# Kernel tuning notes

Measured on AMD Instinct MI355X. Metric: run time of the kernel, lower is better.

## Reference

```python
import jax, jax.numpy as jnp
import numpy as np

D_HEAD = 128
N_HEADS = 8
BATCH = 8
SEQ = 1024


def setup_inputs() -> dict:
    key = jax.random.key(0)
    ks = jax.random.split(key, 11)
    d, nh = D_HEAD, N_HEADS
    D = nh * d
    s_in = 1.0 / np.sqrt(d)   # torch Linear default init bound, fan_in=d
    s_out = 1.0 / np.sqrt(D)  # fan_in=D for out_proj
    u = lambda k, shape, s: jax.random.uniform(k, shape, jnp.float32, -s, s)
    return {
        "q": jax.random.normal(ks[0], (BATCH, SEQ, d), jnp.float32),
        "k": jax.random.normal(ks[1], (BATCH, SEQ, d), jnp.float32),
        "v": jax.random.normal(ks[2], (BATCH, SEQ, d), jnp.float32),
        "Wq": u(ks[3], (d, D), s_in), "bq": u(ks[4], (D,), s_in),
        "Wk": u(ks[5], (d, D), s_in), "bk": u(ks[6], (D,), s_in),
        "Wv": u(ks[7], (d, D), s_in), "bv": u(ks[8], (D,), s_in),
        "Wo": u(ks[9], (D, d), s_out), "bo": u(ks[10], (d,), s_out),
    }


def reference(q, k, v, Wq, bq, Wk, bk, Wv, bv, Wo, bo):
    B, T, d_in = q.shape
    S = k.shape[1]
    nh = N_HEADS
    # projections: [B, L, nh*d] -> [B, nh, L, d]
    split = lambda x: x.reshape(x.shape[0], x.shape[1], nh, -1).transpose(0, 2, 1, 3)
    qh = split(q @ Wq + bq)
    kh = split(k @ Wk + bk)
    vh = split(v @ Wv + bv)
    d_head = qh.shape[-1]
    # scaled dot-product scores: [B, nh, T, S]
    scores = jnp.einsum('bhtd,bhsd->bhts', qh, kh) / jnp.sqrt(jnp.float32(d_head))
    # causal mask (future positions -> -inf), matches triu(fill(-inf), 1)
    causal = jnp.triu(jnp.ones((T, S), dtype=bool), 1)
    scores = jnp.where(causal[None, None], -jnp.inf, scores)
    # softmax in float32 then cast back, as the original does
    probs = jax.nn.softmax(scores.astype(jnp.float32), axis=-1).astype(scores.dtype)
    o = jnp.einsum('bhts,bhsd->bhtd', probs, vh)          # [B, nh, T, d]
    o = o.transpose(0, 2, 1, 3).reshape(B, T, nh * d_head)  # [B, T, D]
    return o @ Wo + bo                                     # [B, T, d]
```

## Files before the change

### kernel.cpp

```cpp
#include <hip/hip_runtime.h>
#include <hip/hip_bf16.h>


typedef __attribute__((ext_vector_type(8))) short short8;
typedef __attribute__((ext_vector_type(4))) short short4v;
typedef __attribute__((ext_vector_type(4))) float f32x4;

#define B_   8
#define S_   1024
#define DH_  128
#define NH_  8
#define DM_  1024

#define MFMA16(a, b, c) __builtin_amdgcn_mfma_f32_16x16x32_bf16((a), (b), (c), 0, 0, 0)

#define GLOAD_LDS16(gsrc, ldst)                                              \
  __builtin_amdgcn_global_load_lds(                                          \
      (const __attribute__((address_space(1))) void*)(gsrc),                 \
      (__attribute__((address_space(3))) void*)(ldst), 16, 0, 0)

__device__ __forceinline__ float bf2f(unsigned short u) {
  union { unsigned int i; float f; } x; x.i = ((unsigned int)u) << 16; return x.f;
}
__device__ __forceinline__ unsigned short f2bf(float f) {
  union { float f; unsigned int i; } x; x.f = f;
  unsigned int r = (x.i + 0x7fffu + ((x.i >> 16) & 1u)) >> 16;
  return (unsigned short)r;
}
__device__ __forceinline__ unsigned short f2h(float f) {
  union { _Float16 h; unsigned short u; } x; x.h = (_Float16)f; return x.u;
}
__device__ __forceinline__ float h2f(unsigned short u) {
  union { unsigned short u; _Float16 h; } x; x.u = u; return (float)x.h;
}
__device__ __forceinline__ float ldany(const void* p, int i, int fp) {
  return fp ? ((const float*)p)[i] : bf2f(((const unsigned short*)p)[i]);
}

__global__ void k_detect(const unsigned short* __restrict__ in, int* __restrict__ flag) {
  __shared__ int f;
  int tid = threadIdx.x;
  if (tid == 0) f = 0;
  __syncthreads();
  int t = 0;
  for (int i = tid; i < 16384; i += 256) {
    unsigned h = in[i];
    unsigned e = (h >> 7) & 0xFFu, m = h & 0x7Fu;
    if (e == 0xFFu || (e == 0u && m != 0u)) t = 1;
  }
  if (t) atomicOr(&f, 1);
  __syncthreads();
  if (tid == 0) *flag = f;
}

__global__ void k_cvt_x(const void* __restrict__ q, const void* __restrict__ k,
                        const void* __restrict__ v, const int* __restrict__ flag,
                        unsigned short* __restrict__ Xq, unsigned short* __restrict__ Xk,
                        unsigned short* __restrict__ Xv) {
  const int fp = *flag;
  int z = blockIdx.y;
  const void* in = (z == 0) ? q : (z == 1) ? k : v;
  unsigned short* out = (z == 0) ? Xq : (z == 1) ? Xk : Xv;
  int e4 = (blockIdx.x * 256 + threadIdx.x) * 4;
  if (fp) {
    f32x4 x = *(const f32x4*)&((const float*)in)[e4];
    short4v o;
#pragma unroll
    for (int j = 0; j < 4; ++j) o[j] = (short)f2bf(x[j]);
    *(short4v*)&out[e4] = o;
  } else {
    *(short4v*)&out[e4] = *(const short4v*)&((const unsigned short*)in)[e4];
  }
}

__global__ void k_cvt_w(const void* __restrict__ Wq, const void* __restrict__ Wk,
                        const void* __restrict__ Wv, const void* __restrict__ Wo,
                        const void* __restrict__ bq, const void* __restrict__ bk,
                        const void* __restrict__ bv, const void* __restrict__ bo,
                        const int* __restrict__ flag,
                        unsigned short* __restrict__ wqT, unsigned short* __restrict__ wkT,
                        unsigned short* __restrict__ wvT, unsigned short* __restrict__ woT,
                        unsigned short* __restrict__ bqc, unsigned short* __restrict__ bkc,
                        unsigned short* __restrict__ bvc, unsigned short* __restrict__ boc) {
  const int fp = *flag;
  int g = blockIdx.x * 256 + threadIdx.x;
  if (g < 393216) {
    int z = g >> 17, e = g & 131071;
    const void* in = (z == 0) ? Wq : (z == 1) ? Wk : Wv;
    unsigned short* out = (z == 0) ? wqT : (z == 1) ? wkT : wvT;
    int r = e >> 10, c = e & 1023;
    out[c * 128 + r] = f2bf(ldany(in, e, fp));
  } else if (g < 524288) {
    int e = g - 393216;
    int r = e >> 7, c = e & 127;
    woT[c * 1024 + r] = f2bf(ldany(Wo, e, fp));
  } else if (g < 525312) {
    int e = g - 524288; bqc[e] = f2bf(ldany(bq, e, fp));
  } else if (g < 526336) {
    int e = g - 525312; bkc[e] = f2bf(ldany(bk, e, fp));
  } else if (g < 527360) {
    int e = g - 526336; bvc[e] = f2bf(ldany(bv, e, fp));
  } else if (g < 527488) {
    int e = g - 527360; boc[e] = f2bf(ldany(bo, e, fp));
  }
}

__global__ __launch_bounds__(256) void k_qkv(
    const unsigned short* __restrict__ Xq, const unsigned short* __restrict__ Xk,
    const unsigned short* __restrict__ Xv,
    const unsigned short* __restrict__ WqT, const unsigned short* __restrict__ WkT,
    const unsigned short* __restrict__ WvT,
    const unsigned short* __restrict__ bq, const unsigned short* __restrict__ bk,
    const unsigned short* __restrict__ bv,
    unsigned short* __restrict__ Qp, unsigned short* __restrict__ Kp,
    unsigned short* __restrict__ VpT) {
  __shared__ unsigned short vtile[128][136];

  const int mat = blockIdx.z;
  const unsigned short* X    = (mat == 0) ? Xq  : (mat == 1) ? Xk  : Xv;
  const unsigned short* WT   = (mat == 0) ? WqT : (mat == 1) ? WkT : WvT;
  const unsigned short* bias = (mat == 0) ? bq  : (mat == 1) ? bk  : bv;
  const float scale = (mat == 0) ? (1.4426950408889634f / 11.313708498984761f) : 1.0f;

  const int tid = threadIdx.x, lane = tid & 63, wave = tid >> 6;
  const int wm = wave >> 1, wn = wave & 1;
  const int l15 = lane & 15, lg = lane >> 4;
  const int mbase = blockIdx.x * 128 + wm * 64;
  const int nbase = blockIdx.y * 128 + wn * 64;

  short8 a[4][4];
#pragma unroll
  for (int mi = 0; mi < 4; ++mi)
#pragma unroll
    for (int kk = 0; kk < 4; ++kk)
      a[mi][kk] = *(const short8*)&X[(mbase + mi * 16 + l15) * DH_ + kk * 32 + lg * 8];

  f32x4 acc[4][4];
#pragma unroll
  for (int mi = 0; mi < 4; ++mi)
#pragma unroll
    for (int ni = 0; ni < 4; ++ni) acc[mi][ni] = (f32x4){0.f, 0.f, 0.f, 0.f};

#pragma unroll
  for (int ni = 0; ni < 4; ++ni) {
    short8 bfr[4];
#pragma unroll
    for (int kk = 0; kk < 4; ++kk)
      bfr[kk] = *(const short8*)&WT[(nbase + ni * 16 + l15) * DH_ + kk * 32 + lg * 8];
#pragma unroll
    for (int mi = 0; mi < 4; ++mi)
#pragma unroll
      for (int kk = 0; kk < 4; ++kk)
        acc[mi][ni] = MFMA16(a[mi][kk], bfr[kk], acc[mi][ni]);
  }

  if (mat < 2) {
    unsigned short* Out = (mat == 0) ? Qp : Kp;
#pragma unroll
    for (int mi = 0; mi < 4; ++mi)
#pragma unroll
      for (int ni = 0; ni < 4; ++ni) {
        int n = nbase + ni * 16 + l15;
        float bv_ = bf2f(bias[n]);
        int h = n >> 7, dh = n & 127;
#pragma unroll
        for (int reg = 0; reg < 4; ++reg) {
          int m = mbase + mi * 16 + lg * 4 + reg;
          int b = m >> 10, t = m & 1023;
          float val = (acc[mi][ni][reg] + bv_) * scale;
          Out[((b * NH_ + h) * S_ + t) * DH_ + dh] = f2bf(val);
        }
      }
  } else {
#pragma unroll
    for (int mi = 0; mi < 4; ++mi)
#pragma unroll
      for (int ni = 0; ni < 4; ++ni) {
        int nl = wn * 64 + ni * 16 + l15;
        float bv_ = bf2f(bias[blockIdx.y * 128 + nl]);
#pragma unroll
        for (int reg = 0; reg < 4; ++reg) {
          int ml_ = wm * 64 + mi * 16 + lg * 4 + reg;
          vtile[ml_][nl] = f2bf(acc[mi][ni][reg] + bv_);
        }
      }
    __syncthreads();
    int n = tid >> 1;
    int thalf = (tid & 1) * 64;
    int b = blockIdx.x >> 3;
    int h = blockIdx.y;
    int base = ((b * NH_ + h) * DH_ + n) * S_ + (blockIdx.x & 7) * 128 + thalf;
#pragma unroll
    for (int jj = 0; jj < 8; ++jj) {
      short8 v;
#pragma unroll
      for (int j2 = 0; j2 < 8; ++j2) v[j2] = (short)vtile[thalf + jj * 8 + j2][n];
      *(short8*)&VpT[base + jj * 8] = v;
    }
  }
}

__global__ __launch_bounds__(256) void k_attn_split(
    const unsigned short* __restrict__ Qp, const unsigned short* __restrict__ Kp,
    const unsigned short* __restrict__ VpT,
    unsigned short* __restrict__ Opart, float* __restrict__ ml,
    unsigned short* __restrict__ O) {
  __shared__ __align__(16) unsigned short kbuf[2][4096];
  __shared__ __align__(16) unsigned short vbuf[2][4096];
  __shared__ __align__(16) unsigned short plds[4][16][44];

  const int tid = threadIdx.x, lane = tid & 63, w = tid >> 6;
  const int l15 = lane & 15, lg = lane >> 4;

  const int bid = blockIdx.x;
  const int swz = (bid & 7) * 320 + (bid >> 3);
  const int bh = swz / 40;
  const int bj = 39 - (swz % 40);
  int G, c;
  if (bj < 4)       { G = bj;                  c = 0; }
  else if (bj < 12) { G = 4 + ((bj - 4) >> 1); c = (bj - 4) & 1; }
  else if (bj < 24) { G = 8 + (bj - 12) / 3;   c = (bj - 12) % 3; }
  else              { G = 12 + ((bj - 24) >> 2); c = (bj - 24) & 3; }
  const int qw = 4 * G + w;
  const int q0 = qw * 16;
  const int cd = G >> 2;
  const bool dia = (c == cd);
  const int sbeg = c * 256;
  const int nt_w   = dia ? ((qw >> 1) + 1 - 8 * c) : 8;
  const int nt_blk = dia ? (2 * G + 2 - 8 * c) : 8;

  const unsigned short* Qb = Qp + bh * (S_ * DH_);
  const unsigned short* Kb = Kp + bh * (S_ * DH_);
  const unsigned short* Vb = VpT + bh * (DH_ * S_);

  const int krow4 = lane >> 4;
  const int kslot = lane & 15;
  const int vd16  = lane >> 2;
  const int vslot = lane & 3;

#define STAGE(bb, sb_) do {                                                        \
    int r0_ = w * 8 + krow4;                                                       \
    GLOAD_LDS16(Kb + ((sb_) + r0_) * DH_ + ((kslot ^ (r0_ & 7)) * 8),              \
                &kbuf[bb][(w * 8) * 128]);                                         \
    int r1_ = w * 8 + 4 + krow4;                                                   \
    GLOAD_LDS16(Kb + ((sb_) + r1_) * DH_ + ((kslot ^ (r1_ & 7)) * 8),              \
                &kbuf[bb][(w * 8 + 4) * 128]);                                     \
    int d0_ = w * 32 + vd16;                                                       \
    GLOAD_LDS16(Vb + d0_ * S_ + (sb_) + vslot * 8, &vbuf[bb][(w * 32) * 32]);      \
    int d1_ = w * 32 + 16 + vd16;                                                  \
    GLOAD_LDS16(Vb + d1_ * S_ + (sb_) + vslot * 8, &vbuf[bb][(w * 32 + 16) * 32]); \
  } while (0)

  short8 qf[4];
#pragma unroll
  for (int kk = 0; kk < 4; ++kk)
    qf[kk] = *(const short8*)&Qb[(q0 + l15) * DH_ + kk * 32 + lg * 8];

  short8 ones;
#pragma unroll
  for (int jj = 0; jj < 8; ++jj) ones[jj] = (short)0x3F80;

  f32x4 of[8], l_acc;
  float m_[4];
#pragma unroll
  for (int di = 0; di < 8; ++di) of[di] = (f32x4){0.f, 0.f, 0.f, 0.f};
  l_acc = (f32x4){0.f, 0.f, 0.f, 0.f};
#pragma unroll
  for (int reg = 0; reg < 4; ++reg) m_[reg] = -1e30f;

  STAGE(0, sbeg);
  __syncthreads();

  for (int kt = 0; kt < nt_blk; ++kt) {
    const int cb = kt & 1;
    if (kt + 1 < nt_blk) STAGE(cb ^ 1, sbeg + (kt + 1) * 32);

    if (kt < nt_w) {
      const int sb = sbeg + kt * 32;
      const int xsl = l15 & 7;

      f32x4 s0 = (f32x4){0.f, 0.f, 0.f, 0.f}, s1 = (f32x4){0.f, 0.f, 0.f, 0.f};
#pragma unroll
      for (int kk = 0; kk < 4; ++kk) {
        short8 kf0 = *(const short8*)&kbuf[cb][l15 * 128 + (((kk * 4 + lg) ^ xsl) * 8)];
        short8 kf1 = *(const short8*)&kbuf[cb][(16 + l15) * 128 + (((kk * 4 + lg) ^ xsl) * 8)];
        s0 = MFMA16(qf[kk], kf0, s0);
        s1 = MFMA16(qf[kk], kf1, s1);
      }

      if (dia && kt == nt_w - 1) {
        const int qrow = q0 + lg * 4;
#pragma unroll
        for (int reg = 0; reg < 4; ++reg) {
          if (sb + l15 > qrow + reg)      s0[reg] = -1e30f;
          if (sb + 16 + l15 > qrow + reg) s1[reg] = -1e30f;
        }
      }

      bool need = false;
      float vmax[4];
#pragma unroll
      for (int reg = 0; reg < 4; ++reg) {
        vmax[reg] = fmaxf(s0[reg], s1[reg]);
        need |= (vmax[reg] > m_[reg] + 8.0f);
      }
      if (__any(need)) {
        float alpha[4];
#pragma unroll
        for (int reg = 0; reg < 4; ++reg) {
          float rm = vmax[reg];
#pragma unroll
          for (int d = 1; d < 16; d <<= 1) rm = fmaxf(rm, __shfl_xor(rm, d));
          float mn = fmaxf(m_[reg], rm);
          alpha[reg] = __builtin_amdgcn_exp2f(m_[reg] - mn);
          m_[reg] = mn;
        }
#pragma unroll
        for (int di = 0; di < 8; ++di)
#pragma unroll
          for (int reg = 0; reg < 4; ++reg) of[di][reg] *= alpha[reg];
#pragma unroll
        for (int reg = 0; reg < 4; ++reg) l_acc[reg] *= alpha[reg];
      }

#pragma unroll
      for (int reg = 0; reg < 4; ++reg) {
        float p0 = __builtin_amdgcn_exp2f(s0[reg] - m_[reg]);
        float p1 = __builtin_amdgcn_exp2f(s1[reg] - m_[reg]);
        union { float f; unsigned int i; } u0, u1;
        u0.f = p0; u1.f = p1;
        plds[w][lg * 4 + reg][l15]      = (unsigned short)((u0.i + 0x8000u) >> 16);
        plds[w][lg * 4 + reg][16 + l15] = (unsigned short)((u1.i + 0x8000u) >> 16);
      }

      short8 pa = *(const short8*)&plds[w][l15][lg * 8];

#pragma unroll
      for (int di = 0; di < 8; ++di) {
        short8 vfd = *(const short8*)&vbuf[cb][(di * 16 + l15) * 32 + lg * 8];
        of[di] = MFMA16(pa, vfd, of[di]);
      }
      l_acc = MFMA16(pa, ones, l_acc);
    }
    __syncthreads();
  }

  if (qw < 16) {
    const int b = bh >> 3, h = bh & 7;
#pragma unroll
    for (int reg = 0; reg < 4; ++reg) {
      int row = lg * 4 + reg;
      float inv = 1.0f / l_acc[reg];
      int qq = q0 + row;
#pragma unroll
      for (int di = 0; di < 8; ++di)
        O[(b * S_ + qq) * DM_ + h * DH_ + di * 16 + l15] = f2bf(of[di][reg] * inv);
    }
  } else {
    int runit;
    if (qw < 32)      runit = 16 + 2 * (qw - 16) + c;
    else if (qw < 48) runit = 48 + 3 * (qw - 32) + c;
    else              runit = 96 + 4 * (qw - 48) + c;
    const int g = bh * 160 + runit;
    unsigned short* op = Opart + g * 2048;
    float* mlg = ml + g * 32;
#pragma unroll
    for (int reg = 0; reg < 4; ++reg) {
      int row = lg * 4 + reg;
      float inv = 1.0f / l_acc[reg];
#pragma unroll
      for (int di = 0; di < 8; ++di)
        op[row * 128 + di * 16 + l15] = f2h(of[di][reg] * inv);
      if (l15 == 0) {
        mlg[row * 2]     = m_[reg];
        mlg[row * 2 + 1] = l_acc[reg];
      }
    }
  }
#undef STAGE
}

__global__ void k_combine(const unsigned short* __restrict__ Opart,
                          const float* __restrict__ ml,
                          unsigned short* __restrict__ O) {
  const int bh = blockIdx.x / 48, qw = 16 + blockIdx.x % 48;
  const int nc = (qw >> 4) + 1;
  const int rbase = (qw < 32) ? 16 + 2 * (qw - 16)
                  : (qw < 48) ? 48 + 3 * (qw - 32)
                              : 96 + 4 * (qw - 48);
  const int g0 = bh * 160 + rbase;
  const int tid = threadIdx.x;
  const int row = tid >> 4, d0 = (tid & 15) * 8;

  float m[4], l[4];
  float mx = -1e30f;
  for (int i = 0; i < nc; ++i) {
    m[i] = ml[(g0 + i) * 32 + row * 2];
    l[i] = ml[(g0 + i) * 32 + row * 2 + 1];
    mx = fmaxf(mx, m[i]);
  }
  float wt[4], wsum = 0.f;
  for (int i = 0; i < nc; ++i) { wt[i] = l[i] * exp2f(m[i] - mx); wsum += wt[i]; }
  float invw = 1.0f / wsum;

  float acc[8];
#pragma unroll
  for (int jj = 0; jj < 8; ++jj) acc[jj] = 0.f;
  for (int i = 0; i < nc; ++i) {
    short8 v = *(const short8*)&Opart[(g0 + i) * 2048 + row * 128 + d0];
    float wgt = wt[i];
#pragma unroll
    for (int jj = 0; jj < 8; ++jj) acc[jj] += wgt * h2f((unsigned short)v[jj]);
  }

  const int b = bh >> 3, h = bh & 7;
  const int qq = qw * 16 + row;
  short8 o;
#pragma unroll
  for (int jj = 0; jj < 8; ++jj) o[jj] = (short)f2bf(acc[jj] * invw);
  *(short8*)&O[(b * S_ + qq) * DM_ + h * DH_ + d0] = o;
}

__global__ __launch_bounds__(256) void k_attn(
    const unsigned short* __restrict__ Qp, const unsigned short* __restrict__ Kp,
    const unsigned short* __restrict__ VpT, unsigned short* __restrict__ O) {
  __shared__ __align__(16) unsigned short plds[4][2][16][44];

  const int qt = 7 - blockIdx.x;
  const int bh = blockIdx.y;
  const int tid = threadIdx.x, lane = tid & 63, w = tid >> 6;
  const int l15 = lane & 15, lg = lane >> 4;
  const int q0 = qt * 128 + w * 32;

  const unsigned short* Qb = Qp + bh * (S_ * DH_);
  const unsigned short* Kb = Kp + bh * (S_ * DH_);
  const unsigned short* Vb = VpT + bh * (DH_ * S_);

  short8 qf[2][4];
#pragma unroll
  for (int mi = 0; mi < 2; ++mi)
#pragma unroll
    for (int kk = 0; kk < 4; ++kk)
      qf[mi][kk] = *(const short8*)&Qb[(q0 + mi * 16 + l15) * DH_ + kk * 32 + lg * 8];

  f32x4 of[2][8];
  float m_[2][4], l_[2][4];
#pragma unroll
  for (int mi = 0; mi < 2; ++mi) {
#pragma unroll
    for (int di = 0; di < 8; ++di) of[mi][di] = (f32x4){0.f, 0.f, 0.f, 0.f};
#pragma unroll
    for (int reg = 0; reg < 4; ++reg) { m_[mi][reg] = -1e30f; l_[mi][reg] = 0.f; }
  }

  const int ntiles = q0 / 32 + 1;
  for (int kt = 0; kt < ntiles; ++kt) {
    const int sb = kt * 32;
    const bool lastt = (kt == ntiles - 1);

    f32x4 s[2][2];
#pragma unroll
    for (int mi = 0; mi < 2; ++mi)
#pragma unroll
      for (int ni = 0; ni < 2; ++ni) s[mi][ni] = (f32x4){0.f, 0.f, 0.f, 0.f};
#pragma unroll
    for (int ni = 0; ni < 2; ++ni) {
      short8 kf[4];
#pragma unroll
      for (int kk = 0; kk < 4; ++kk)
        kf[kk] = *(const short8*)&Kb[(sb + ni * 16 + l15) * DH_ + kk * 32 + lg * 8];
#pragma unroll
      for (int mi = 0; mi < 2; ++mi)
#pragma unroll
        for (int kk = 0; kk < 4; ++kk)
          s[mi][ni] = MFMA16(qf[mi][kk], kf[kk], s[mi][ni]);
    }

#pragma unroll
    for (int mi = 0; mi < 2; ++mi) {
      float alpha[4];
#pragma unroll
      for (int reg = 0; reg < 4; ++reg) {
        int q = q0 + mi * 16 + lg * 4 + reg;
        float v0 = s[mi][0][reg];
        float v1 = s[mi][1][reg];
        if (lastt) {
          if (sb + l15 > q)      v0 = -1e30f;
          if (sb + 16 + l15 > q) v1 = -1e30f;
        }
        float rmax = fmaxf(v0, v1);
#pragma unroll
        for (int d = 1; d < 16; d <<= 1) rmax = fmaxf(rmax, __shfl_xor(rmax, d));
        float mn = fmaxf(m_[mi][reg], rmax);
        alpha[reg] = __builtin_amdgcn_exp2f(m_[mi][reg] - mn);
        m_[mi][reg] = mn;
        float p0 = __builtin_amdgcn_exp2f(v0 - mn), p1 = __builtin_amdgcn_exp2f(v1 - mn);
        float rs = p0 + p1;
#pragma unroll
        for (int d = 1; d < 16; d <<= 1) rs += __shfl_xor(rs, d);
        l_[mi][reg] = l_[mi][reg] * alpha[reg] + rs;
        plds[w][mi][lg * 4 + reg][l15]      = f2bf(p0);
        plds[w][mi][lg * 4 + reg][16 + l15] = f2bf(p1);
      }
#pragma unroll
      for (int di = 0; di < 8; ++di)
#pragma unroll
        for (int reg = 0; reg < 4; ++reg) of[mi][di][reg] *= alpha[reg];
    }

    short8 pa[2];
#pragma unroll
    for (int mi = 0; mi < 2; ++mi)
      pa[mi] = *(const short8*)&plds[w][mi][l15][lg * 8];

#pragma unroll
    for (int di = 0; di < 8; ++di) {
      short8 vf = *(const short8*)&Vb[(di * 16 + l15) * S_ + sb + lg * 8];
#pragma unroll
      for (int mi = 0; mi < 2; ++mi) of[mi][di] = MFMA16(pa[mi], vf, of[mi][di]);
    }
  }

  const int b = bh >> 3, h = bh & 7;
#pragma unroll
  for (int mi = 0; mi < 2; ++mi)
#pragma unroll
    for (int reg = 0; reg < 4; ++reg) {
      float inv = 1.0f / l_[mi][reg];
      int q = q0 + mi * 16 + lg * 4 + reg;
#pragma unroll
      for (int di = 0; di < 8; ++di) {
        int d = di * 16 + l15;
        O[(b * S_ + q) * DM_ + h * DH_ + d] = f2bf(of[mi][di][reg] * inv);
      }
    }
}

__global__ __launch_bounds__(256) void k_oproj(
    const unsigned short* __restrict__ O, const unsigned short* __restrict__ WoT,
    float* __restrict__ outacc) {
  const int tid = threadIdx.x, lane = tid & 63, wave = tid >> 6;
  const int wm = wave >> 1, wn = wave & 1;
  const int l15 = lane & 15, lg = lane >> 4;
  const int mbase = blockIdx.x * 128 + wm * 64;
  const int kc = blockIdx.y;

  f32x4 acc[4][4];
#pragma unroll
  for (int mi = 0; mi < 4; ++mi)
#pragma unroll
    for (int ni = 0; ni < 4; ++ni) acc[mi][ni] = (f32x4){0.f, 0.f, 0.f, 0.f};

  for (int ks = 0; ks < 8; ++ks) {
    int kb = kc * 256 + ks * 32;
    short8 a[4], bfr[4];
#pragma unroll
    for (int mi = 0; mi < 4; ++mi)
      a[mi] = *(const short8*)&O[(mbase + mi * 16 + l15) * DM_ + kb + lg * 8];
#pragma unroll
    for (int ni = 0; ni < 4; ++ni)
      bfr[ni] = *(const short8*)&WoT[(wn * 64 + ni * 16 + l15) * DM_ + kb + lg * 8];
#pragma unroll
    for (int mi = 0; mi < 4; ++mi)
#pragma unroll
      for (int ni = 0; ni < 4; ++ni) acc[mi][ni] = MFMA16(a[mi], bfr[ni], acc[mi][ni]);
  }

  float* oa = outacc + kc * (8192 * 128);
#pragma unroll
  for (int mi = 0; mi < 4; ++mi)
#pragma unroll
    for (int ni = 0; ni < 4; ++ni) {
      int n = wn * 64 + ni * 16 + l15;
#pragma unroll
      for (int reg = 0; reg < 4; ++reg) {
        int m = mbase + mi * 16 + lg * 4 + reg;
        oa[m * 128 + n] = acc[mi][ni][reg];
      }
    }
}

__global__ void k_final(const float* __restrict__ outacc,
                        const unsigned short* __restrict__ boc,
                        const int* __restrict__ flag, void* __restrict__ out) {
  int i4 = (blockIdx.x * 256 + threadIdx.x) * 4;
  f32x4 v = *(const f32x4*)&outacc[i4];
  v += *(const f32x4*)&outacc[1048576 + i4];
  v += *(const f32x4*)&outacc[2097152 + i4];
  v += *(const f32x4*)&outacc[3145728 + i4];
  int n0 = i4 & 127;
#pragma unroll
  for (int j = 0; j < 4; ++j) v[j] += bf2f(boc[n0 + j]);
  if (*flag) {
    *(f32x4*)&((float*)out)[i4] = v;
  } else {
    short4v o;
#pragma unroll
    for (int j = 0; j < 4; ++j) o[j] = (short)f2bf(v[j]);
    *(short4v*)&((unsigned short*)out)[i4] = o;
  }
}

extern "C" void kernel_launch(void* const* d_in, const int* in_sizes, int n_in,
                              void* d_out, int out_size, void* d_ws, size_t ws_size,
                              hipStream_t stream) {
  const void* q  = d_in[0];
  const void* k  = d_in[1];
  const void* v  = d_in[2];
  const void* Wq = d_in[3];
  const void* bq = d_in[4];
  const void* Wk = d_in[5];
  const void* bk = d_in[6];
  const void* Wv = d_in[7];
  const void* bv = d_in[8];
  const void* Wo = d_in[9];
  const void* bo = d_in[10];

  char* ws = (char*)d_ws;
  int*            flag = (int*)(ws + 0);
  unsigned short* wqT  = (unsigned short*)(ws + 4096);
  unsigned short* wkT  = (unsigned short*)(ws + 266240);
  unsigned short* wvT  = (unsigned short*)(ws + 528384);
  unsigned short* woT  = (unsigned short*)(ws + 790528);
  unsigned short* bqc  = (unsigned short*)(ws + 1052672);
  unsigned short* bkc  = (unsigned short*)(ws + 1054720);
  unsigned short* bvc  = (unsigned short*)(ws + 1056768);
  unsigned short* boc  = (unsigned short*)(ws + 1058816);
  unsigned short* Xq   = (unsigned short*)(ws + 2097152);
  unsigned short* Xk   = (unsigned short*)(ws + 4194304);
  unsigned short* Xv   = (unsigned short*)(ws + 6291456);
  unsigned short* Qp   = (unsigned short*)(ws + 8388608);
  unsigned short* Kp   = (unsigned short*)(ws + 25165824);
  unsigned short* VpT  = (unsigned short*)(ws + 41943040);
  unsigned short* O    = (unsigned short*)(ws + 58720256);
  float*          oacc = (float*)(ws + 75497472);
  unsigned short* Opart= (unsigned short*)(ws + 75497472);
  float*          ml   = (float*)(ws + 2097152);

  const bool use_split = ws_size >= (size_t)117440512;

  k_detect<<<dim3(1), 256, 0, stream>>>((const unsigned short*)q, flag);
  k_cvt_x<<<dim3(1024, 3), 256, 0, stream>>>(q, k, v, flag, Xq, Xk, Xv);
  k_cvt_w<<<dim3(2061), 256, 0, stream>>>(Wq, Wk, Wv, Wo, bq, bk, bv, bo, flag,
                                          wqT, wkT, wvT, woT, bqc, bkc, bvc, boc);
  k_qkv<<<dim3(64, 8, 3), 256, 0, stream>>>(Xq, Xk, Xv, wqT, wkT, wvT, bqc, bkc, bvc,
                                            Qp, Kp, VpT);
  if (use_split) {
    k_attn_split<<<dim3(2560), 256, 0, stream>>>(Qp, Kp, VpT, Opart, ml, O);
    k_combine<<<dim3(3072), 256, 0, stream>>>(Opart, ml, O);
  } else {
    k_attn<<<dim3(8, 64), 256, 0, stream>>>(Qp, Kp, VpT, O);
  }
  k_oproj<<<dim3(64, 4), 256, 0, stream>>>(O, woT, oacc);
  k_final<<<dim3(1024), 256, 0, stream>>>(oacc, boc, flag, d_out);
}
```

Measured before the change: 142.5 us.

## Stage Q/K projection output through LDS, prefetch weights, set MFMA priority

The QKV projection now writes every matrix's biased and scaled tile into shared memory and stores Q/K with 16-byte coalesced vector writes, replacing scattered 2-byte global stores. Weight fragments are double-buffered so the next column group loads while the current MFMAs run. The attention kernels raise wave priority around MFMA loops with s_setprio, and the P staging row pitch changes from 44 to 48 elements. This adds a barrier and LDS traffic to the Q/K path, and the new pitch may change LDS bank conflicts.

Result: no change. 144.6 us (+1.5%).

```diff
diff --git a/kernel.cpp b/kernel.cpp
--- a/kernel.cpp
+++ b/kernel.cpp
@@ -114,7 +114,7 @@
     const unsigned short* __restrict__ bv,
     unsigned short* __restrict__ Qp, unsigned short* __restrict__ Kp,
     unsigned short* __restrict__ VpT) {
-  __shared__ unsigned short vtile[128][136];
+  __shared__ __align__(16) unsigned short vtile[128][136];
 
   const int mat = blockIdx.z;
   const unsigned short* X    = (mat == 0) ? Xq  : (mat == 1) ? Xk  : Xv;
@@ -141,54 +141,55 @@
 #pragma unroll
     for (int ni = 0; ni < 4; ++ni) acc[mi][ni] = (f32x4){0.f, 0.f, 0.f, 0.f};
 
+  short8 bfr[2][4];
+#pragma unroll
+  for (int kk = 0; kk < 4; ++kk)
+    bfr[0][kk] = *(const short8*)&WT[(nbase + l15) * DH_ + kk * 32 + lg * 8];
+
 #pragma unroll
   for (int ni = 0; ni < 4; ++ni) {
-    short8 bfr[4];
-#pragma unroll
-    for (int kk = 0; kk < 4; ++kk)
-      bfr[kk] = *(const short8*)&WT[(nbase + ni * 16 + l15) * DH_ + kk * 32 + lg * 8];
+    if (ni < 3) {
+#pragma unroll
+      for (int kk = 0; kk < 4; ++kk)
+        bfr[(ni + 1) & 1][kk] =
+            *(const short8*)&WT[(nbase + (ni + 1) * 16 + l15) * DH_ + kk * 32 + lg * 8];
+    }
 #pragma unroll
     for (int mi = 0; mi < 4; ++mi)
 #pragma unroll
       for (int kk = 0; kk < 4; ++kk)
-        acc[mi][ni] = MFMA16(a[mi][kk], bfr[kk], acc[mi][ni]);
-  }
-
+        acc[mi][ni] = MFMA16(a[mi][kk], bfr[ni & 1][kk], acc[mi][ni]);
+  }
+
+#pragma unroll
+  for (int mi = 0; mi < 4; ++mi)
+#pragma unroll
+    for (int ni = 0; ni < 4; ++ni) {
+      int nl = wn * 64 + ni * 16 + l15;
+      float bv_ = bf2f(bias[blockIdx.y * 128 + nl]);
+#pragma unroll
+      for (int reg = 0; reg < 4; ++reg) {
+        int ml_ = wm * 64 + mi * 16 + lg * 4 + reg;
+        vtile[ml_][nl] = f2bf((acc[mi][ni][reg] + bv_) * scale);
+      }
+    }
+  __syncthreads();
+
+  const int b = blockIdx.x >> 3;
+  const int h = blockIdx.y;
   if (mat < 2) {
-    unsigned short* Out = (mat == 0) ? Qp : Kp;
-#pragma unroll
-    for (int mi = 0; mi < 4; ++mi)
-#pragma unroll
-      for (int ni = 0; ni < 4; ++ni) {
-        int n = nbase + ni * 16 + l15;
-        float bv_ = bf2f(bias[n]);
-        int h = n >> 7, dh = n & 127;
-#pragma unroll
-        for (int reg = 0; reg < 4; ++reg) {
-          int m = mbase + mi * 16 + lg * 4 + reg;
-          int b = m >> 10, t = m & 1023;
-          float val = (acc[mi][ni][reg] + bv_) * scale;
-          Out[((b * NH_ + h) * S_ + t) * DH_ + dh] = f2bf(val);
-        }
-      }
+    unsigned short* Out = ((mat == 0) ? Qp : Kp) +
+        ((b * NH_ + h) * S_ + (blockIdx.x & 7) * 128) * DH_;
+#pragma unroll
+    for (int j = 0; j < 8; ++j) {
+      int r = j * 16 + (tid >> 4);
+      int c0 = (tid & 15) * 8;
+      short8 v = *(const short8*)&vtile[r][c0];
+      *(short8*)&Out[j * 2048 + tid * 8] = v;
+    }
   } else {
-#pragma unroll
-    for (int mi = 0; mi < 4; ++mi)
-#pragma unroll
-      for (int ni = 0; ni < 4; ++ni) {
-        int nl = wn * 64 + ni * 16 + l15;
-        float bv_ = bf2f(bias[blockIdx.y * 128 + nl]);
-#pragma unroll
-        for (int reg = 0; reg < 4; ++reg) {
-          int ml_ = wm * 64 + mi * 16 + lg * 4 + reg;
-          vtile[ml_][nl] = f2bf(acc[mi][ni][reg] + bv_);
-        }
-      }
-    __syncthreads();
     int n = tid >> 1;
     int thalf = (tid & 1) * 64;
-    int b = blockIdx.x >> 3;
-    int h = blockIdx.y;
     int base = ((b * NH_ + h) * DH_ + n) * S_ + (blockIdx.x & 7) * 128 + thalf;
 #pragma unroll
     for (int jj = 0; jj < 8; ++jj) {
@@ -207,7 +208,7 @@
     unsigned short* __restrict__ O) {
   __shared__ __align__(16) unsigned short kbuf[2][4096];
   __shared__ __align__(16) unsigned short vbuf[2][4096];
-  __shared__ __align__(16) unsigned short plds[4][16][44];
+  __shared__ __align__(16) unsigned short plds[4][16][48];
 
   const int tid = threadIdx.x, lane = tid & 63, w = tid >> 6;
   const int l15 = lane & 15, lg = lane >> 4;
@@ -280,6 +281,7 @@
       const int xsl = l15 & 7;
 
       f32x4 s0 = (f32x4){0.f, 0.f, 0.f, 0.f}, s1 = (f32x4){0.f, 0.f, 0.f, 0.f};
+      __builtin_amdgcn_s_setprio(1);
 #pragma unroll
       for (int kk = 0; kk < 4; ++kk) {
         short8 kf0 = *(const short8*)&kbuf[cb][l15 * 128 + (((kk * 4 + lg) ^ xsl) * 8)];
@@ -287,6 +289,7 @@
         s0 = MFMA16(qf[kk], kf0, s0);
         s1 = MFMA16(qf[kk], kf1, s1);
       }
+      __builtin_amdgcn_s_setprio(0);
 
       if (dia && kt == nt_w - 1) {
         const int qrow = q0 + lg * 4;
@@ -335,12 +338,14 @@
 
       short8 pa = *(const short8*)&plds[w][l15][lg * 8];
 
+      __builtin_amdgcn_s_setprio(1);
 #pragma unroll
       for (int di = 0; di < 8; ++di) {
         short8 vfd = *(const short8*)&vbuf[cb][(di * 16 + l15) * 32 + lg * 8];
         of[di] = MFMA16(pa, vfd, of[di]);
       }
       l_acc = MFMA16(pa, ones, l_acc);
+      __builtin_amdgcn_s_setprio(0);
     }
     __syncthreads();
   }
@@ -424,7 +429,7 @@
 __global__ __launch_bounds__(256) void k_attn(
     const unsigned short* __restrict__ Qp, const unsigned short* __restrict__ Kp,
     const unsigned short* __restrict__ VpT, unsigned short* __restrict__ O) {
-  __shared__ __align__(16) unsigned short plds[4][2][16][44];
+  __shared__ __align__(16) unsigned short plds[4][2][16][48];
 
   const int qt = 7 - blockIdx.x;
   const int bh = blockIdx.y;
```
